# Kernel optimization log

Measured on AMD Instinct MI355X. Metric: run time of the kernel, lower is better.

Reference implementation:

```python
import jax, jax.numpy as jnp
import numpy as np

D_MODEL = 1024
NUM_HEADS = 16
HEAD_DIM = D_MODEL // NUM_HEADS
B, S = 4, 2048


def setup_inputs() -> dict:
    key = jax.random.key(0)
    ks = jax.random.split(key, 12)
    s = 1.0 / np.sqrt(D_MODEL)
    return {
        "inputs_q": jax.random.normal(ks[0], (B, S, D_MODEL), jnp.float32),
        "inputs_k": jax.random.normal(ks[1], (B, S, D_MODEL), jnp.float32),
        "inputs_v": jax.random.normal(ks[2], (B, S, D_MODEL), jnp.float32),
        "Wq": jax.random.normal(ks[3], (D_MODEL, D_MODEL), jnp.float32) * s,
        "bq": jax.random.normal(ks[4], (D_MODEL,), jnp.float32) * 0.01,
        "Wk": jax.random.normal(ks[5], (D_MODEL, D_MODEL), jnp.float32) * s,
        "bk": jax.random.normal(ks[6], (D_MODEL,), jnp.float32) * 0.01,
        "Wv": jax.random.normal(ks[7], (D_MODEL, D_MODEL), jnp.float32) * s,
        "bv": jax.random.normal(ks[8], (D_MODEL,), jnp.float32) * 0.01,
        "Wo": jax.random.normal(ks[9], (D_MODEL, D_MODEL), jnp.float32) * s,
        "bo": jax.random.normal(ks[10], (D_MODEL,), jnp.float32) * 0.01,
    }


def reference(inputs_q, inputs_k, inputs_v, Wq, bq, Wk, bk, Wv, bv, Wo, bo):
    b, s, _ = inputs_q.shape
    # linear projections
    q = inputs_q @ Wq + bq  # [b, s, d_model]
    k = inputs_k @ Wk + bk
    v = inputs_v @ Wv + bv
    # split heads: bsd -> bhsd
    q = q.reshape(b, s, NUM_HEADS, HEAD_DIM).transpose(0, 2, 1, 3)
    k = k.reshape(b, s, NUM_HEADS, HEAD_DIM).transpose(0, 2, 1, 3)
    v = v.reshape(b, s, NUM_HEADS, HEAD_DIM).transpose(0, 2, 1, 3)
    scale = 1.0 / jnp.sqrt(jnp.asarray(HEAD_DIM, q.dtype))
    scores = jnp.einsum('bhqd,bhkd->bhqk', q, k) * scale  # [b,h,s,s]
    # causal mask: position q attends to k <= q
    causal = jnp.tril(jnp.ones((s, s), dtype=bool))
    scores = jnp.where(causal[None, None], scores, jnp.asarray(-jnp.inf, scores.dtype))
    attn = jax.nn.softmax(scores, axis=-1)
    ctx = jnp.einsum('bhqk,bhkd->bhqd', attn, v)  # [b,h,s,hd]
    ctx = ctx.transpose(0, 2, 1, 3).reshape(b, s, D_MODEL)
    return ctx @ Wo + bo
```

## Files before the change

### kernel.cpp

```cpp
#include <hip/hip_runtime.h>
#include <math.h>
#include <type_traits>

typedef __bf16 bf16;
typedef __attribute__((ext_vector_type(8))) __bf16 bf16x8;
typedef __attribute__((ext_vector_type(4))) float f32x4;

#define SEQ 2048
#define DM 1024
#define NH 16
#define HD 64
#define BATCH 4

#define NEG_BIG (-1e30f)
#define SCALE_L2E 0.18033688011f

__device__ inline bf16x8 cvt_f32x8(const float* p) {
  f32x4 x0 = *(const f32x4*)p;
  f32x4 x1 = *(const f32x4*)(p + 4);
  bf16x8 r;
  r[0] = (bf16)x0[0]; r[1] = (bf16)x0[1]; r[2] = (bf16)x0[2]; r[3] = (bf16)x0[3];
  r[4] = (bf16)x1[0]; r[5] = (bf16)x1[1]; r[6] = (bf16)x1[2]; r[7] = (bf16)x1[3];
  return r;
}

__global__ __launch_bounds__(256) void transpose_w_kernel(
    const float* __restrict__ Wq, const float* __restrict__ Wk,
    const float* __restrict__ Wv, const float* __restrict__ Wo,
    bf16* __restrict__ Tq, bf16* __restrict__ Tk,
    bf16* __restrict__ Tv, bf16* __restrict__ To) {
  __shared__ bf16 tile[64 * 66];
  int z = blockIdx.z;
  const float* src = (z == 0) ? Wq : (z == 1) ? Wk : (z == 2) ? Wv : Wo;
  bf16* dst = (z == 0) ? Tq : (z == 1) ? Tk : (z == 2) ? Tv : To;
  int n0 = blockIdx.x * 64, k0 = blockIdx.y * 64;
  int t = threadIdx.x;
  int c = t & 63, rr = t >> 6;
#pragma unroll
  for (int i = 0; i < 16; i++) {
    int k = i * 4 + rr;
    tile[k * 66 + c] = (bf16)src[(size_t)(k0 + k) * DM + n0 + c];
  }
  __syncthreads();
#pragma unroll
  for (int i = 0; i < 16; i++) {
    int n = i * 4 + rr;
    dst[(size_t)(n0 + n) * DM + k0 + c] = tile[c * 66 + n];
  }
}

__global__ __launch_bounds__(256) void transpose_v_kernel(
    const bf16* __restrict__ Vn, bf16* __restrict__ Vt) {
  __shared__ bf16 tile[64 * 66];
  int s0 = blockIdx.x * 64;
  int h = blockIdx.y, b = blockIdx.z;
  int t = threadIdx.x;
  int c = t & 63, rr = t >> 6;
#pragma unroll
  for (int i = 0; i < 16; i++) {
    int s = i * 4 + rr;
    tile[s * 66 + c] = Vn[((size_t)(b * SEQ + s0 + s)) * DM + h * HD + c];
  }
  __syncthreads();
#pragma unroll
  for (int i = 0; i < 16; i++) {
    int d = i * 4 + rr;
    Vt[((size_t)(b * NH + h) * HD + d) * SEQ + s0 + c] = tile[c * 66 + d];
  }
}

template <typename AT, typename CT>
__global__ __launch_bounds__(256) void gemm_bias_kernel(
    const AT* __restrict__ A, const bf16* __restrict__ Bt,
    const float* __restrict__ bias, CT* __restrict__ C) {
  __shared__ bf16 As[4 * 128 * 8];
  __shared__ bf16 Bs[4 * 128 * 8];
  int m0 = blockIdx.x * 128, n0 = blockIdx.y * 128;
  int t = threadIdx.x;
  int wave = t >> 6, lane = t & 63, lr = lane & 15, lq = lane >> 4;
  int wm = (wave & 1) * 64, wn = (wave >> 1) * 64;

  f32x4 acc[4][4];
#pragma unroll
  for (int i = 0; i < 4; i++)
#pragma unroll
    for (int j = 0; j < 4; j++) acc[i][j] = (f32x4){0.f, 0.f, 0.f, 0.f};

  int rA = t >> 2;
  int kcA = t & 3;
  const AT* pa = A + (size_t)(m0 + rA) * DM + kcA * 8;
  const bf16* pb = Bt + (size_t)(n0 + rA) * DM + kcA * 8;

  for (int k0 = 0; k0 < DM; k0 += 32) {
    bf16x8 a0, a1;
    if constexpr (std::is_same_v<AT, float>) {
      a0 = cvt_f32x8(pa);
      a1 = cvt_f32x8(pa + (size_t)64 * DM);
    } else {
      a0 = *(const bf16x8*)(pa);
      a1 = *(const bf16x8*)(pa + (size_t)64 * DM);
    }
    bf16x8 b0 = *(const bf16x8*)(pb);
    bf16x8 b1 = *(const bf16x8*)(pb + (size_t)64 * DM);
    pa += 32;
    pb += 32;
    *(bf16x8*)&As[(kcA * 128 + rA) * 8] = a0;
    *(bf16x8*)&As[(kcA * 128 + rA + 64) * 8] = a1;
    *(bf16x8*)&Bs[(kcA * 128 + rA) * 8] = b0;
    *(bf16x8*)&Bs[(kcA * 128 + rA + 64) * 8] = b1;
    __syncthreads();

    bf16x8 af[4], bfr[4];
#pragma unroll
    for (int i = 0; i < 4; i++)
      af[i] = *(const bf16x8*)&As[(lq * 128 + wm + i * 16 + lr) * 8];
#pragma unroll
    for (int j = 0; j < 4; j++)
      bfr[j] = *(const bf16x8*)&Bs[(lq * 128 + wn + j * 16 + lr) * 8];
#pragma unroll
    for (int i = 0; i < 4; i++)
#pragma unroll
      for (int j = 0; j < 4; j++)
        acc[i][j] = __builtin_amdgcn_mfma_f32_16x16x32_bf16(af[i], bfr[j],
                                                            acc[i][j], 0, 0, 0);
    __syncthreads();
  }

#pragma unroll
  for (int j = 0; j < 4; j++) {
    int col = n0 + wn + j * 16 + lr;
    float bv = bias[col];
#pragma unroll
    for (int i = 0; i < 4; i++) {
      int row = m0 + wm + i * 16 + lq * 4;
#pragma unroll
      for (int r = 0; r < 4; r++) {
        C[(size_t)(row + r) * DM + col] = (CT)(acc[i][j][r] + bv);
      }
    }
  }
}

__global__ __launch_bounds__(256, 2) void attention_kernel(
    const bf16* __restrict__ Q, const bf16* __restrict__ K,
    const bf16* __restrict__ Vt, bf16* __restrict__ ctx) {
  int h = blockIdx.y, b = blockIdx.z;
  int t = threadIdx.x, wave = t >> 6, lane = t & 63, lr = lane & 15,
      lq = lane >> 4;
  int p = blockIdx.x * 4 + wave;

  const bf16* Qb = Q + (size_t)b * SEQ * DM + h * HD;
  const bf16* Kb = K + (size_t)b * SEQ * DM + h * HD;
  const bf16* Vb = Vt + (size_t)(b * NH + h) * HD * SEQ;
  bf16* Cb = ctx + (size_t)b * SEQ * DM + h * HD;

#pragma unroll 1
  for (int pass = 0; pass < 2; pass++) {
    int tq = pass ? (63 - p) : p;
    int q0 = tq * 32;

    bf16x8 qf[2][2];
#pragma unroll
    for (int qi = 0; qi < 2; qi++)
#pragma unroll
      for (int ks = 0; ks < 2; ks++)
        qf[qi][ks] = *(const bf16x8*)&Qb[(size_t)(q0 + qi * 16 + lr) * DM +
                                         ks * 32 + lq * 8];

    f32x4 o[2][4];
    float m_st[2], l_st[2];
#pragma unroll
    for (int mi = 0; mi < 2; mi++) {
#pragma unroll
      for (int dj = 0; dj < 4; dj++) o[mi][dj] = (f32x4){0.f, 0.f, 0.f, 0.f};
      m_st[mi] = NEG_BIG;
      l_st[mi] = 0.f;
    }

    int kv_end = q0 + 32;
#pragma unroll 1
    for (int kv0 = 0; kv0 < kv_end; kv0 += 64) {
      bf16x8 kf[4][2];
#pragma unroll
      for (int kvt = 0; kvt < 4; kvt++)
#pragma unroll
        for (int ks = 0; ks < 2; ks++)
          kf[kvt][ks] = *(const bf16x8*)&Kb[(size_t)(kv0 + kvt * 16 + lr) * DM +
                                            ks * 32 + lq * 8];
      bf16x8 vf[4][2];
#pragma unroll
      for (int dj = 0; dj < 4; dj++)
#pragma unroll
        for (int ks2 = 0; ks2 < 2; ks2++)
          vf[dj][ks2] = *(const bf16x8*)&Vb[(size_t)(dj * 16 + lr) * SEQ + kv0 +
                                            ks2 * 32 + lq * 8];

      f32x4 s[4][2];
#pragma unroll
      for (int kvt = 0; kvt < 4; kvt++)
#pragma unroll
        for (int qi = 0; qi < 2; qi++) {
          f32x4 acc = (f32x4){0.f, 0.f, 0.f, 0.f};
          acc = __builtin_amdgcn_mfma_f32_16x16x32_bf16(kf[kvt][0], qf[qi][0],
                                                        acc, 0, 0, 0);
          acc = __builtin_amdgcn_mfma_f32_16x16x32_bf16(kf[kvt][1], qf[qi][1],
                                                        acc, 0, 0, 0);
          s[kvt][qi] = acc;
        }

      if (kv0 + 63 > q0) {
#pragma unroll
        for (int kvt = 0; kvt < 4; kvt++)
#pragma unroll
          for (int qi = 0; qi < 2; qi++)
#pragma unroll
            for (int r = 0; r < 4; r++) {
              int kv_g = kv0 + kvt * 16 + lq * 4 + r;
              int q_g = q0 + qi * 16 + lr;
              float v = s[kvt][qi][r] * SCALE_L2E;
              s[kvt][qi][r] = (kv_g > q_g) ? NEG_BIG : v;
            }
      } else {
#pragma unroll
        for (int kvt = 0; kvt < 4; kvt++)
#pragma unroll
          for (int qi = 0; qi < 2; qi++)
#pragma unroll
            for (int r = 0; r < 4; r++) s[kvt][qi][r] *= SCALE_L2E;
      }

      float alpha[2];
#pragma unroll
      for (int qi = 0; qi < 2; qi++) {
        float mx = s[0][qi][0];
#pragma unroll
        for (int kvt = 0; kvt < 4; kvt++)
#pragma unroll
          for (int r = 0; r < 4; r++) mx = fmaxf(mx, s[kvt][qi][r]);
        mx = fmaxf(mx, __shfl_xor(mx, 16));
        mx = fmaxf(mx, __shfl_xor(mx, 32));
        float mnew = fmaxf(m_st[qi], mx);
        alpha[qi] = exp2f(m_st[qi] - mnew);
        m_st[qi] = mnew;
        float rs = 0.f;
#pragma unroll
        for (int kvt = 0; kvt < 4; kvt++)
#pragma unroll
          for (int r = 0; r < 4; r++) {
            float pv = exp2f(s[kvt][qi][r] - mnew);
            s[kvt][qi][r] = pv;
            rs += pv;
          }
        rs += __shfl_xor(rs, 16);
        rs += __shfl_xor(rs, 32);
        l_st[qi] = l_st[qi] * alpha[qi] + rs;
      }

      float aT[2][4];
#pragma unroll
      for (int mi = 0; mi < 2; mi++)
#pragma unroll
        for (int r = 0; r < 4; r++) aT[mi][r] = __shfl(alpha[mi], lq * 4 + r);
#pragma unroll
      for (int mi = 0; mi < 2; mi++)
#pragma unroll
        for (int dj = 0; dj < 4; dj++)
#pragma unroll
          for (int r = 0; r < 4; r++) o[mi][dj][r] *= aT[mi][r];

      int src_base = (lq & 1) * 32 + lr;
      bool hi = (lq >> 1) != 0;
#pragma unroll
      for (int ks2 = 0; ks2 < 2; ks2++) {
        bf16x8 pf[2];
#pragma unroll
        for (int mi = 0; mi < 2; mi++) {
#pragma unroll
          for (int j = 0; j < 8; j++) {
            int src = src_base + (j >> 2) * 16;
            float v0 = __shfl(s[2 * ks2][mi][j & 3], src);
            float v1 = __shfl(s[2 * ks2 + 1][mi][j & 3], src);
            pf[mi][j] = (bf16)(hi ? v1 : v0);
          }
        }
#pragma unroll
        for (int dj = 0; dj < 4; dj++) {
          o[0][dj] = __builtin_amdgcn_mfma_f32_16x16x32_bf16(pf[0], vf[dj][ks2],
                                                             o[0][dj], 0, 0, 0);
          o[1][dj] = __builtin_amdgcn_mfma_f32_16x16x32_bf16(pf[1], vf[dj][ks2],
                                                             o[1][dj], 0, 0, 0);
        }
      }
    }

    float lT[2][4];
#pragma unroll
    for (int mi = 0; mi < 2; mi++)
#pragma unroll
      for (int r = 0; r < 4; r++)
        lT[mi][r] = 1.f / __shfl(l_st[mi], lq * 4 + r);
#pragma unroll
    for (int mi = 0; mi < 2; mi++)
#pragma unroll
      for (int r = 0; r < 4; r++) {
        int row = q0 + mi * 16 + lq * 4 + r;
#pragma unroll
        for (int dj = 0; dj < 4; dj++)
          Cb[(size_t)row * DM + dj * 16 + lr] = (bf16)(o[mi][dj][r] * lT[mi][r]);
      }
  }
}

extern "C" void kernel_launch(void* const* d_in, const int* in_sizes, int n_in,
                              void* d_out, int out_size, void* d_ws,
                              size_t ws_size, hipStream_t stream) {
  const float* iq = (const float*)d_in[0];
  const float* ik = (const float*)d_in[1];
  const float* iv = (const float*)d_in[2];
  const float* Wq = (const float*)d_in[3];
  const float* bq = (const float*)d_in[4];
  const float* Wk = (const float*)d_in[5];
  const float* bk = (const float*)d_in[6];
  const float* Wv = (const float*)d_in[7];
  const float* bv = (const float*)d_in[8];
  const float* Wo = (const float*)d_in[9];
  const float* bo = (const float*)d_in[10];

  char* ws = (char*)d_ws;
  const size_t MB = 1024 * 1024;
  bf16* Tq = (bf16*)(ws + 0 * MB);
  bf16* Tk = (bf16*)(ws + 2 * MB);
  bf16* Tv = (bf16*)(ws + 4 * MB);
  bf16* To = (bf16*)(ws + 6 * MB);
  bf16* Qp = (bf16*)(ws + 8 * MB);
  bf16* Kp = (bf16*)(ws + 24 * MB);
  bf16* Vp = (bf16*)(ws + 40 * MB);
  bf16* Vtp = (bf16*)d_out;
  bf16* Cx = Vp;

  transpose_w_kernel<<<dim3(16, 16, 4), 256, 0, stream>>>(Wq, Wk, Wv, Wo, Tq,
                                                          Tk, Tv, To);
  gemm_bias_kernel<float, bf16><<<dim3(64, 8), 256, 0, stream>>>(iq, Tq, bq, Qp);
  gemm_bias_kernel<float, bf16><<<dim3(64, 8), 256, 0, stream>>>(ik, Tk, bk, Kp);
  gemm_bias_kernel<float, bf16><<<dim3(64, 8), 256, 0, stream>>>(iv, Tv, bv, Vp);
  transpose_v_kernel<<<dim3(32, 16, 4), 256, 0, stream>>>(Vp, Vtp);
  attention_kernel<<<dim3(8, 16, 4), 256, 0, stream>>>(Qp, Kp, Vtp, Cx);
  gemm_bias_kernel<bf16, float><<<dim3(64, 8), 256, 0, stream>>>(
      Cx, To, bo, (float*)d_out);
}
```

Baseline: 453.8 us.

## Stage GEMM tiles via direct global-to-LDS loads and pre-convert fp32 inputs

The projection GEMMs now fill shared memory with global_load_lds 16-byte transfers straight from global memory, skipping the trip through registers. The shared tiles change to a row-major 128x32 layout so each wave's direct-copy destination is contiguous. Because direct LDS copies cannot convert fp32 to bf16, a new elementwise kernel converts each fp32 activation input to bf16 in scratch space before its GEMM. That adds three extra kernel launches and a full extra read and write of each input. Correctness relies on the barrier waiting for the async copies to land, and the new LDS layout may cause more bank conflicts on the fragment reads.

```diff
diff --git a/kernel.cpp b/kernel.cpp
--- a/kernel.cpp
+++ b/kernel.cpp
@@ -22,6 +22,18 @@
   r[0] = (bf16)x0[0]; r[1] = (bf16)x0[1]; r[2] = (bf16)x0[2]; r[3] = (bf16)x0[3];
   r[4] = (bf16)x1[0]; r[5] = (bf16)x1[1]; r[6] = (bf16)x1[2]; r[7] = (bf16)x1[3];
   return r;
+}
+
+__device__ inline void async_copy16(const bf16* g, bf16* l) {
+  __builtin_amdgcn_global_load_lds(
+      (const __attribute__((address_space(1))) unsigned int*)g,
+      (__attribute__((address_space(3))) unsigned int*)l, 16, 0, 0);
+}
+
+__global__ __launch_bounds__(256) void cvt_kernel(const float* __restrict__ src,
+                                                  bf16* __restrict__ dst) {
+  size_t i = ((size_t)blockIdx.x * 256 + threadIdx.x) * 8;
+  *(bf16x8*)(dst + i) = cvt_f32x8(src + i);
 }
 
 __global__ __launch_bounds__(256) void transpose_w_kernel(
@@ -69,12 +81,12 @@
   }
 }
 
-template <typename AT, typename CT>
+template <typename CT>
 __global__ __launch_bounds__(256) void gemm_bias_kernel(
-    const AT* __restrict__ A, const bf16* __restrict__ Bt,
+    const bf16* __restrict__ A, const bf16* __restrict__ Bt,
     const float* __restrict__ bias, CT* __restrict__ C) {
-  __shared__ bf16 As[4 * 128 * 8];
-  __shared__ bf16 Bs[4 * 128 * 8];
+  __shared__ bf16 As[128 * 32];
+  __shared__ bf16 Bs[128 * 32];
   int m0 = blockIdx.x * 128, n0 = blockIdx.y * 128;
   int t = threadIdx.x;
   int wave = t >> 6, lane = t & 63, lr = lane & 15, lq = lane >> 4;
@@ -86,37 +98,32 @@
 #pragma unroll
     for (int j = 0; j < 4; j++) acc[i][j] = (f32x4){0.f, 0.f, 0.f, 0.f};
 
-  int rA = t >> 2;
-  int kcA = t & 3;
-  const AT* pa = A + (size_t)(m0 + rA) * DM + kcA * 8;
-  const bf16* pb = Bt + (size_t)(n0 + rA) * DM + kcA * 8;
+  int srow = wave * 32 + (lane >> 2);
+  int skc = lane & 3;
+  const bf16* gA0 = A + (size_t)(m0 + srow) * DM + skc * 8;
+  const bf16* gA1 = gA0 + (size_t)16 * DM;
+  const bf16* gB0 = Bt + (size_t)(n0 + srow) * DM + skc * 8;
+  const bf16* gB1 = gB0 + (size_t)16 * DM;
+  bf16* lA0 = &As[(wave * 128) * 8];
+  bf16* lA1 = &As[(wave * 128 + 64) * 8];
+  bf16* lB0 = &Bs[(wave * 128) * 8];
+  bf16* lB1 = &Bs[(wave * 128 + 64) * 8];
 
   for (int k0 = 0; k0 < DM; k0 += 32) {
-    bf16x8 a0, a1;
-    if constexpr (std::is_same_v<AT, float>) {
-      a0 = cvt_f32x8(pa);
-      a1 = cvt_f32x8(pa + (size_t)64 * DM);
-    } else {
-      a0 = *(const bf16x8*)(pa);
-      a1 = *(const bf16x8*)(pa + (size_t)64 * DM);
-    }
-    bf16x8 b0 = *(const bf16x8*)(pb);
-    bf16x8 b1 = *(const bf16x8*)(pb + (size_t)64 * DM);
-    pa += 32;
-    pb += 32;
-    *(bf16x8*)&As[(kcA * 128 + rA) * 8] = a0;
-    *(bf16x8*)&As[(kcA * 128 + rA + 64) * 8] = a1;
-    *(bf16x8*)&Bs[(kcA * 128 + rA) * 8] = b0;
-    *(bf16x8*)&Bs[(kcA * 128 + rA + 64) * 8] = b1;
+    async_copy16(gA0, lA0);
+    async_copy16(gA1, lA1);
+    async_copy16(gB0, lB0);
+    async_copy16(gB1, lB1);
+    gA0 += 32; gA1 += 32; gB0 += 32; gB1 += 32;
     __syncthreads();
 
     bf16x8 af[4], bfr[4];
 #pragma unroll
     for (int i = 0; i < 4; i++)
-      af[i] = *(const bf16x8*)&As[(lq * 128 + wm + i * 16 + lr) * 8];
+      af[i] = *(const bf16x8*)&As[(wm + i * 16 + lr) * 32 + lq * 8];
 #pragma unroll
     for (int j = 0; j < 4; j++)
-      bfr[j] = *(const bf16x8*)&Bs[(lq * 128 + wn + j * 16 + lr) * 8];
+      bfr[j] = *(const bf16x8*)&Bs[(wn + j * 16 + lr) * 32 + lq * 8];
 #pragma unroll
     for (int i = 0; i < 4; i++)
 #pragma unroll
@@ -335,16 +342,20 @@
   bf16* Qp = (bf16*)(ws + 8 * MB);
   bf16* Kp = (bf16*)(ws + 24 * MB);
   bf16* Vp = (bf16*)(ws + 40 * MB);
+  bf16* X = (bf16*)d_out;
   bf16* Vtp = (bf16*)d_out;
   bf16* Cx = Vp;
 
   transpose_w_kernel<<<dim3(16, 16, 4), 256, 0, stream>>>(Wq, Wk, Wv, Wo, Tq,
                                                           Tk, Tv, To);
-  gemm_bias_kernel<float, bf16><<<dim3(64, 8), 256, 0, stream>>>(iq, Tq, bq, Qp);
-  gemm_bias_kernel<float, bf16><<<dim3(64, 8), 256, 0, stream>>>(ik, Tk, bk, Kp);
-  gemm_bias_kernel<float, bf16><<<dim3(64, 8), 256, 0, stream>>>(iv, Tv, bv, Vp);
+  cvt_kernel<<<dim3(4096), 256, 0, stream>>>(iq, X);
+  gemm_bias_kernel<bf16><<<dim3(64, 8), 256, 0, stream>>>(X, Tq, bq, Qp);
+  cvt_kernel<<<dim3(4096), 256, 0, stream>>>(ik, X);
+  gemm_bias_kernel<bf16><<<dim3(64, 8), 256, 0, stream>>>(X, Tk, bk, Kp);
+  cvt_kernel<<<dim3(4096), 256, 0, stream>>>(iv, X);
+  gemm_bias_kernel<bf16><<<dim3(64, 8), 256, 0, stream>>>(X, Tv, bv, Vp);
   transpose_v_kernel<<<dim3(32, 16, 4), 256, 0, stream>>>(Vp, Vtp);
   attention_kernel<<<dim3(8, 16, 4), 256, 0, stream>>>(Qp, Kp, Vtp, Cx);
-  gemm_bias_kernel<bf16, float><<<dim3(64, 8), 256, 0, stream>>>(
-      Cx, To, bo, (float*)d_out);
-}
+  gemm_bias_kernel<float><<<dim3(64, 8), 256, 0, stream>>>(Cx, To, bo,
+                                                           (float*)d_out);
+}
```

Result: faster. 402.1 us (-11.4%).
